# Kernel optimization log

Hardware: AMD Instinct MI355X
Metric: run time of the kernel (lower is better)

Reference implementation:

```python
import jax, jax.numpy as jnp
import numpy as np
import math

B = 128        # batch (= bipartite matching N)
L = 16         # detector layers (MAX_LAYER)
E = 768        # n_embd
D = E // 2     # RFF target_dim
H = 12         # n_head
HD = E // H    # head_size
NL = 6         # n_layer
SEQ = 12       # tokens after concats: 3+3 -> 6 -> +currentLayer -> 12
MAX_LAYER = L
LN_EPS = 1e-3  # keras LayerNormalization default


def setup_inputs() -> dict:
    key = jax.random.key(0)
    ks = jax.random.split(key, 8)
    inp = {}
    inp["X"] = jax.random.normal(ks[0], (B, L, 3), dtype=jnp.float32) * 50.0
    inp["targets"] = jax.random.normal(ks[1], (B, L, 3), dtype=jnp.float32)
    # RandomFourierFeatures params (random per-call in original; fixed here):
    # x: xmin=-160,xmax=160,n=9*1024 ; y: n=12*512 ; dE: xmin=0,xmax=230,n=2300
    specs = [(-160.0, 160.0, 9 * 1024), (-160.0, 160.0, 12 * 512), (0.0, 230.0, 2300)]
    om, ph = [], []
    for i, (xmin, xmax, n) in enumerate(specs):
        k1, k2 = jax.random.split(jax.random.fold_in(ks[2], i))
        omin = 2.0 * math.pi / (xmax - xmin)
        lo, hi = math.log(omin / n), math.log(omin)
        om.append(jnp.exp(jax.random.uniform(k1, (D,), minval=lo, maxval=hi)))
        ph.append(jax.random.uniform(k2, (D,)))  # B ~ U(0,1)*scale, scale=1
    inp["omegas"] = jnp.stack(om).astype(jnp.float32)  # (3, D)
    inp["phases"] = jnp.stack(ph).astype(jnp.float32)  # (3, D)
    # np.random.permutation per layer-step, fixed here
    inp["perms"] = jnp.stack(
        [jax.random.permutation(jax.random.fold_in(ks[3], i), B) for i in range(L - 1)]
    ).astype(jnp.int32)  # (L-1, B)
    # transformer weights (stacked over layers)
    kk = jax.random.split(ks[4], 16)
    s = 0.02
    inp["Wq"] = jax.random.normal(kk[0], (NL, E, H, HD)) * s
    inp["bq"] = jnp.zeros((NL, H, HD))
    inp["Wk"] = jax.random.normal(kk[1], (NL, E, H, HD)) * s
    inp["bk"] = jnp.zeros((NL, H, HD))
    inp["Wv"] = jax.random.normal(kk[2], (NL, E, H, HD)) * s
    inp["bv"] = jnp.zeros((NL, H, HD))
    inp["Wo"] = jax.random.normal(kk[3], (NL, H, HD, E)) * s
    inp["bo"] = jnp.zeros((NL, E))
    inp["ln1g"] = jnp.ones((NL, E)); inp["ln1b"] = jnp.zeros((NL, E))
    inp["ln2g"] = jnp.ones((NL, E)); inp["ln2b"] = jnp.zeros((NL, E))
    inp["W1"] = jax.random.normal(kk[4], (NL, E, 4 * E)) * s
    inp["b1f"] = jnp.zeros((NL, 4 * E))
    inp["W2"] = jax.random.normal(kk[5], (NL, 4 * E, E)) * s
    inp["b2f"] = jnp.zeros((NL, E))
    inp["lnfg"] = jnp.ones((E,)); inp["lnfb"] = jnp.zeros((E,))
    inp["Wout"] = jax.random.normal(kk[6], (SEQ * E, 3)) * s
    inp["bout"] = jnp.zeros((3,))
    return inp


def _ln(x, g, b):
    mu = jnp.mean(x, -1, keepdims=True)
    v = jnp.var(x, -1, keepdims=True)
    return (x - mu) * jax.lax.rsqrt(v + LN_EPS) * g + b


def _greedy_match(cost):
    """Greedy bipartite matching: sort all NxN costs ascending, assign first-come.
    Returns row_to_col_match_vec (N,) int32."""
    N = cost.shape[0]
    order = jnp.argsort(cost.reshape(-1))

    def step(carry, k):
        row, col = carry
        i = k // N
        j = k % N
        ok = (row[i] == -1) & (col[j] == -1)
        row = row.at[i].set(jnp.where(ok, j, row[i]))
        col = col.at[j].set(jnp.where(ok, i, col[j]))
        return (row, col), None

    init = (jnp.full((N,), -1, jnp.int32), jnp.full((N,), -1, jnp.int32))
    (row, _), _ = jax.lax.scan(step, init, order)
    return row


def _forward(X, targets, omegas, phases, perms, Wq, bq, Wk, bk, Wv, bv, Wo, bo,
             ln1g, ln1b, ln2g, ln2b, W1, b1f, W2, b2f, lnfg, lnfb, Wout, bout):
    # RFF: (B,L,3) -> (B,L,3,D)
    XS = jnp.cos(X[..., None] * omegas[None, None, :, :] + phases[None, None, :, :])
    losses = []
    scale = 1.0 / math.sqrt(HD)
    for lidx in range(1, L):
        xc = XS[:, -lidx]        # (B,3,D)
        xp = XS[:, -lidx - 1]    # (B,3,D)
        x = jnp.concatenate([xc, xp], axis=2)            # (B,3,E)
        y = targets[:, -lidx + 1]                        # (B,3)
        y_prev = jnp.broadcast_to(y[:, :, None], (B, 3, E))
        x = jnp.concatenate([x, y_prev], axis=1)         # (B,6,E)
        cur = jnp.full_like(x, float(MAX_LAYER - lidx))
        x = jnp.concatenate([x, cur], axis=1)            # (B,12,E)
        x = x[perms[lidx - 1]]                           # batch permutation
        for l in range(NL):
            h = _ln(x, ln1g[l], ln1b[l])
            q = jnp.einsum('bse,ehd->bshd', h, Wq[l]) + bq[l]
            k = jnp.einsum('bse,ehd->bshd', h, Wk[l]) + bk[l]
            v = jnp.einsum('bse,ehd->bshd', h, Wv[l]) + bv[l]
            att = jax.nn.softmax(jnp.einsum('bqhd,bkhd->bhqk', q, k) * scale, axis=-1)
            o = jnp.einsum('bhqk,bkhd->bqhd', att, v)
            x = x + (jnp.einsum('bqhd,hde->bqe', o, Wo[l]) + bo[l])
            h = _ln(x, ln2g[l], ln2b[l])
            x = x + (jnp.maximum(h @ W1[l] + b1f[l], 0.0) @ W2[l] + b2f[l])
        x = _ln(x, lnfg, lnfb).reshape(B, SEQ * E)
        logits = x @ Wout + bout                         # (B,3)
        tgt = targets[:, -lidx]                          # (B,3)
        cost = jnp.sqrt(jnp.sum((logits[:, None, :] - tgt[None, :, :]) ** 2, axis=-1) + 1e-12)
        m = _greedy_match(jax.lax.stop_gradient(cost))
        lm = logits[m]                                   # gather per original
        losses.append(jnp.mean((lm - tgt) ** 2))
    return jnp.mean(jnp.stack(losses))


def reference(X, targets, omegas, phases, perms, Wq, bq, Wk, bk, Wv, bv, Wo, bo,
              ln1g, ln1b, ln2g, ln2b, W1, b1f, W2, b2f, lnfg, lnfb, Wout, bout):
    return _forward(X, targets, omegas, phases, perms, Wq, bq, Wk, bk, Wv, bv, Wo, bo,
                    ln1g, ln1b, ln2g, ln2b, W1, b1f, W2, b2f, lnfg, lnfb, Wout, bout)
```

## Files before the change

kernel.cpp:

```cpp
#include <hip/hip_runtime.h>
#include <hip/hip_bf16.h>
#include <math.h>

#define B_   128
#define L_   16
#define E_   768
#define D_   384
#define H_   12
#define HD_  64
#define NL_  6
#define SEQ_ 12
#define LN_EPS 0.001f
#define WLS   7077888
#define BQS   2304

typedef __attribute__((ext_vector_type(8))) short bf16x8;
typedef __attribute__((ext_vector_type(4))) float f32x4;
typedef unsigned long long u64;

#define GLOAD_LDS16(g, l) \
    __builtin_amdgcn_global_load_lds((__attribute__((address_space(1))) const void*)(g), \
                                     (__attribute__((address_space(3))) void*)(l), 16, 0, 0)

__global__ __launch_bounds__(256) void k_x0(const float* __restrict__ X,
                                            const float* __restrict__ targets,
                                            const int* __restrict__ perms,
                                            const float* __restrict__ om,
                                            const float* __restrict__ ph,
                                            float* __restrict__ x, int cb, int ntok) {
    int i = blockIdx.x * 256 + threadIdx.x;
    if (i >= ntok*E_) return;
    int e   = i % E_;
    int tok = i / E_;
    int s   = tok % SEQ_;
    int bi  = (tok / SEQ_) % B_;
    int c   = tok / (SEQ_*B_);
    int cl  = cb + c;
    int lidx = cl + 1;
    int pb  = perms[cl*B_ + bi];
    float val;
    if (s < 3) {
        int t  = (e < D_) ? (L_ - lidx) : (L_ - lidx - 1);
        int dd = (e < D_) ? e : (e - D_);
        float xv = X[(pb*L_ + t)*3 + s];
        val = cosf(xv * om[s*D_ + dd] + ph[s*D_ + dd]);
    } else if (s < 6) {
        int t = (17 - lidx) & 15;
        val = targets[(pb*L_ + t)*3 + (s - 3)];
    } else {
        val = (float)(L_ - lidx);
    }
    x[i] = val;
}

__global__ __launch_bounds__(256) void k_ln(const float* __restrict__ x,
                                            const float* __restrict__ g,
                                            const float* __restrict__ b,
                                            __hip_bfloat16* __restrict__ h) {
    int gi = blockIdx.x * 256 + threadIdx.x;
    int tok = gi >> 6, lane = gi & 63;
    const float4* xr = (const float4*)(x + (size_t)tok * E_);
    float4 v0 = xr[lane], v1 = xr[lane + 64], v2 = xr[lane + 128];
    float s = v0.x+v0.y+v0.z+v0.w + v1.x+v1.y+v1.z+v1.w + v2.x+v2.y+v2.z+v2.w;
    #pragma unroll
    for (int o = 32; o > 0; o >>= 1) s += __shfl_xor(s, o, 64);
    float mu = s * (1.0f / E_);
    v0.x-=mu; v0.y-=mu; v0.z-=mu; v0.w-=mu;
    v1.x-=mu; v1.y-=mu; v1.z-=mu; v1.w-=mu;
    v2.x-=mu; v2.y-=mu; v2.z-=mu; v2.w-=mu;
    float q = v0.x*v0.x+v0.y*v0.y+v0.z*v0.z+v0.w*v0.w
            + v1.x*v1.x+v1.y*v1.y+v1.z*v1.z+v1.w*v1.w
            + v2.x*v2.x+v2.y*v2.y+v2.z*v2.z+v2.w*v2.w;
    #pragma unroll
    for (int o = 32; o > 0; o >>= 1) q += __shfl_xor(q, o, 64);
    float rstd = rsqrtf(q * (1.0f / E_) + LN_EPS);
    const float4* g4 = (const float4*)g;
    const float4* b4 = (const float4*)b;
    ushort4* h4 = (ushort4*)(h + (size_t)tok * E_);
    #pragma unroll
    for (int k = 0; k < 3; k++) {
        float4 v = (k == 0) ? v0 : (k == 1) ? v1 : v2;
        float4 gg = g4[lane + k*64], bb = b4[lane + k*64];
        ushort4 o;
        o.x = __bfloat16_as_ushort(__float2bfloat16(v.x * rstd * gg.x + bb.x));
        o.y = __bfloat16_as_ushort(__float2bfloat16(v.y * rstd * gg.y + bb.y));
        o.z = __bfloat16_as_ushort(__float2bfloat16(v.z * rstd * gg.z + bb.z));
        o.w = __bfloat16_as_ushort(__float2bfloat16(v.w * rstd * gg.w + bb.w));
        h4[lane + k*64] = o;
    }
}

__global__ __launch_bounds__(256) void k_cvt(const float* __restrict__ Wq,
                                             const float* __restrict__ Wk,
                                             const float* __restrict__ Wv,
                                             const float* __restrict__ Wo,
                                             const float* __restrict__ W1,
                                             const float* __restrict__ W2,
                                             const float* __restrict__ bq,
                                             const float* __restrict__ bk,
                                             const float* __restrict__ bv,
                                             __hip_bfloat16* __restrict__ wl0,
                                             float* __restrict__ bqkv0, int lbase) {
    int bid = blockIdx.x;
    int l   = lbase + bid / 6913;
    bid %= 6913;
    __hip_bfloat16* wl = wl0 + (size_t)(l - lbase) * WLS;
    float* bqkv = bqkv0 + (l - lbase) * BQS;
    int tid = threadIdx.x;
    if (bid == 6912) {
        for (int i = tid; i < 2304; i += 256) {
            float v = (i < 768) ? bq[l*768 + i] : (i < 1536) ? bk[l*768 + i - 768]
                                                             : bv[l*768 + i - 1536];
            bqkv[i] = v;
        }
        return;
    }
    const float* src; __hip_bfloat16* dst; int K, N, ti, tj;
    if (bid < 1728) {
        int part = bid / 576, idx = bid % 576;
        const float* srcs[3] = {Wq, Wk, Wv};
        src = srcs[part] + (size_t)l*768*768; dst = wl + (size_t)part*768*768;
        K = 768; N = 768; tj = idx % 24; ti = idx / 24;
    } else if (bid < 2304) {
        int idx = bid - 1728;
        src = Wo + (size_t)l*768*768; dst = wl + 1769472;
        K = 768; N = 768; tj = idx % 24; ti = idx / 24;
    } else if (bid < 4608) {
        int idx = bid - 2304;
        src = W1 + (size_t)l*768*3072; dst = wl + 2359296;
        K = 768; N = 3072; tj = idx % 96; ti = idx / 96;
    } else {
        int idx = bid - 4608;
        src = W2 + (size_t)l*3072*768; dst = wl + 4718592;
        K = 3072; N = 768; tj = idx % 24; ti = idx / 24;
    }
    __shared__ float tbuf[32][33];
    int tx = tid & 31, ty = tid >> 5;
    #pragma unroll
    for (int p = 0; p < 4; p++) {
        int k = ti*32 + ty + p*8, n = tj*32 + tx;
        tbuf[ty + p*8][tx] = src[(size_t)k*N + n];
    }
    __syncthreads();
    #pragma unroll
    for (int p = 0; p < 4; p++) {
        int n = tj*32 + ty + p*8, k = ti*32 + tx;
        dst[(size_t)n*K + k] = __float2bfloat16(tbuf[tx][ty + p*8]);
    }
}

#define MFMA_BF16(a, b, c) __builtin_amdgcn_mfma_f32_16x16x32_bf16(a, b, c, 0, 0, 0)

__global__ __launch_bounds__(512) void k_gemm256(const __hip_bfloat16* __restrict__ A,
                                                 const __hip_bfloat16* __restrict__ Bt,
                                                 const float* __restrict__ bias,
                                                 void* __restrict__ Cp,
                                                 int K, int ldb, int ldc, int flags) {
    __shared__ __align__(16) char smem[131072];
    const int tid  = threadIdx.x;
    const int lane = tid & 63;
    const int wid  = tid >> 6;
    const int wr   = wid >> 2;
    const int wc   = wid & 3;
    const int m0   = blockIdx.y * 256;
    const int n0   = blockIdx.x * 256;
    const int fr   = lane & 15, fkg = lane >> 4, sx = fr & 7;
    const int NT   = K >> 6;

    const int srow = tid >> 3;
    const int skc  = 8 * ((tid & 7) ^ (srow & 7));

    f32x4 acc[8][4] = {};

    auto stage = [&](int kt, int buf) {
        char* base = smem + buf*65536;
        const int kk = kt*64 + skc;
        GLOAD_LDS16(A  + (size_t)(m0 +       srow) * K   + kk, base +         tid*16);
        GLOAD_LDS16(A  + (size_t)(m0 +  64 + srow) * K   + kk, base +  8192 + tid*16);
        GLOAD_LDS16(A  + (size_t)(m0 + 128 + srow) * K   + kk, base + 16384 + tid*16);
        GLOAD_LDS16(A  + (size_t)(m0 + 192 + srow) * K   + kk, base + 24576 + tid*16);
        GLOAD_LDS16(Bt + (size_t)(n0 +       srow) * ldb + kk, base + 32768 + tid*16);
        GLOAD_LDS16(Bt + (size_t)(n0 +  64 + srow) * ldb + kk, base + 40960 + tid*16);
        GLOAD_LDS16(Bt + (size_t)(n0 + 128 + srow) * ldb + kk, base + 49152 + tid*16);
        GLOAD_LDS16(Bt + (size_t)(n0 + 192 + srow) * ldb + kk, base + 57344 + tid*16);
    };
    auto ldA = [&](int buf, int i, int ks) -> bf16x8 {
        int row = wr*128 + i*16 + fr;
        return *(const bf16x8*)(smem + buf*65536 + row*128 + (((ks*4 + fkg) ^ sx) << 4));
    };
    auto ldB = [&](int buf, int j, int ks) -> bf16x8 {
        int row = wc*64 + j*16 + fr;
        return *(const bf16x8*)(smem + buf*65536 + 32768 + row*128 + (((ks*4 + fkg) ^ sx) << 4));
    };

    stage(0, 0);
    __syncthreads();

    for (int kt = 0; kt < NT; ++kt) {
        const int cur = kt & 1;
        if (kt + 1 < NT) stage(kt + 1, cur ^ 1);
        bf16x8 b[4][2];
        #pragma unroll
        for (int j = 0; j < 4; j++) { b[j][0] = ldB(cur, j, 0); b[j][1] = ldB(cur, j, 1); }
        #pragma unroll
        for (int ih = 0; ih < 2; ih++) {
            bf16x8 a[4][2];
            #pragma unroll
            for (int i = 0; i < 4; i++) {
                a[i][0] = ldA(cur, ih*4 + i, 0);
                a[i][1] = ldA(cur, ih*4 + i, 1);
            }
            __builtin_amdgcn_s_setprio(1);
            #pragma unroll
            for (int i = 0; i < 4; i++)
                #pragma unroll
                for (int j = 0; j < 4; j++) {
                    acc[ih*4+i][j] = MFMA_BF16(a[i][0], b[j][0], acc[ih*4+i][j]);
                    acc[ih*4+i][j] = MFMA_BF16(a[i][1], b[j][1], acc[ih*4+i][j]);
                }
            __builtin_amdgcn_s_setprio(0);
        }
        __syncthreads();
    }

    const int colL = lane & 15, rowg = (lane >> 4) * 4;
    #pragma unroll
    for (int i = 0; i < 8; i++) {
        #pragma unroll
        for (int j = 0; j < 4; j++) {
            int col = n0 + wc*64 + j*16 + colL;
            float bv = bias ? bias[col] : 0.0f;
            #pragma unroll
            for (int r = 0; r < 4; r++) {
                int row = m0 + wr*128 + i*16 + rowg + r;
                float v = acc[i][j][r] + bv;
                if (flags & 4) v = fmaxf(v, 0.0f);
                size_t off = (size_t)row * ldc + col;
                if (flags & 1)      ((__hip_bfloat16*)Cp)[off] = __float2bfloat16(v);
                else if (flags & 2) ((float*)Cp)[off] += v;
                else                ((float*)Cp)[off] = v;
            }
        }
    }
}

__global__ __launch_bounds__(256) void k_attn(const __hip_bfloat16* __restrict__ qkv,
                                              __hip_bfloat16* __restrict__ o) {
    __shared__ float qs[SEQ_][HD_], ks[SEQ_][HD_], vs[SEQ_][HD_];
    __shared__ float att[SEQ_][SEQ_];
    int blk = blockIdx.x;
    int hh  = blk % H_;
    int cbb = blk / H_;
    int t = threadIdx.x;
    if (t < 96) {
        int s = t >> 3, c = (t & 7) * 8;
        size_t base = (size_t)(cbb*SEQ_ + s) * 2304 + hh*64 + c;
        bf16x8 q8 = *(const bf16x8*)(qkv + base);
        bf16x8 k8 = *(const bf16x8*)(qkv + base + 768);
        bf16x8 v8 = *(const bf16x8*)(qkv + base + 1536);
        #pragma unroll
        for (int j = 0; j < 8; j++) {
            qs[s][c+j] = __uint_as_float((unsigned)(unsigned short)q8[j] << 16);
            ks[s][c+j] = __uint_as_float((unsigned)(unsigned short)k8[j] << 16);
            vs[s][c+j] = __uint_as_float((unsigned)(unsigned short)v8[j] << 16);
        }
    }
    __syncthreads();
    if (t < SEQ_*SEQ_) {
        int qi = t / SEQ_, kj = t % SEQ_;
        float s = 0.f;
        #pragma unroll
        for (int d = 0; d < HD_; d++) s += qs[qi][d] * ks[kj][d];
        att[qi][kj] = s * 0.125f;
    }
    __syncthreads();
    if (t < SEQ_) {
        float mx = -1e30f;
        #pragma unroll
        for (int j = 0; j < SEQ_; j++) mx = fmaxf(mx, att[t][j]);
        float e[SEQ_]; float sum = 0.f;
        #pragma unroll
        for (int j = 0; j < SEQ_; j++) { e[j] = expf(att[t][j] - mx); sum += e[j]; }
        float inv = 1.f / sum;
        #pragma unroll
        for (int j = 0; j < SEQ_; j++) att[t][j] = e[j] * inv;
    }
    __syncthreads();
    for (int i = t; i < SEQ_*HD_; i += 256) {
        int s = i / HD_, d = i % HD_;
        float acc = 0.f;
        #pragma unroll
        for (int j = 0; j < SEQ_; j++) acc += att[s][j] * vs[j][d];
        o[(size_t)(cbb*SEQ_ + s) * 768 + hh*64 + d] = __float2bfloat16(acc);
    }
}

__global__ __launch_bounds__(256) void k_logits(const __hip_bfloat16* __restrict__ hfin,
                                                const float* __restrict__ Wout,
                                                const float* __restrict__ bout,
                                                float* __restrict__ logits, int cb) {
    __shared__ float red[3][256];
    int blk = blockIdx.x;
    int t = threadIdx.x;
    const __hip_bfloat16* row = hfin + (size_t)blk * SEQ_ * E_;
    float a0 = 0.f, a1 = 0.f, a2 = 0.f;
    for (int e = t; e < SEQ_*E_; e += 256) {
        float x = __bfloat162float(row[e]);
        a0 += x * Wout[e*3 + 0]; a1 += x * Wout[e*3 + 1]; a2 += x * Wout[e*3 + 2];
    }
    red[0][t] = a0; red[1][t] = a1; red[2][t] = a2;
    __syncthreads();
    for (int o = 128; o > 0; o >>= 1) {
        if (t < o) { red[0][t] += red[0][t+o]; red[1][t] += red[1][t+o]; red[2][t] += red[2][t+o]; }
        __syncthreads();
    }
    if (t < 3) logits[((size_t)cb*B_ + blk)*3 + t] = red[t][0] + bout[t];
}

__global__ __launch_bounds__(64) void k_match(const float* __restrict__ logits,
                                              const float* __restrict__ targets,
                                              float* __restrict__ losses) {
    __shared__ float cst[128 * 129];
    __shared__ float tg[128][3];
    __shared__ int mrow[128];
    int cl = blockIdx.x, lane = threadIdx.x;
    int lidx = cl + 1;
    for (int j = lane; j < 128; j += 64) {
        const float* tp = &targets[((size_t)j*L_ + (L_ - lidx)) * 3];
        tg[j][0] = tp[0]; tg[j][1] = tp[1]; tg[j][2] = tp[2];
    }
    __syncthreads();
    u64 kc[2];
    #pragma unroll
    for (int hh = 0; hh < 2; hh++) {
        int r = lane + hh*64;
        const float* lg = &logits[(cl*B_ + r) * 3];
        float l0 = lg[0], l1 = lg[1], l2 = lg[2];
        u64 best = ~0ull;
        for (int c = 0; c < 128; c++) {
            float d0 = l0 - tg[c][0], d1 = l1 - tg[c][1], d2 = l2 - tg[c][2];
            float cc = sqrtf(d0*d0 + d1*d1 + d2*d2 + 1e-12f);
            cst[r*129 + c] = cc;
            u64 key = ((u64)__float_as_uint(cc) << 14) | (unsigned)(r*128 + c);
            best = key < best ? key : best;
        }
        kc[hh] = best;
    }
    __syncthreads();
    u64 dead0 = 0, dead1 = 0;
    int done = 0;
    for (int trip = 0; trip < 16640 && done < 128; trip++) {
        u64 b = kc[0] < kc[1] ? kc[0] : kc[1];
        #pragma unroll
        for (int o = 32; o > 0; o >>= 1) {
            u64 x = __shfl_xor(b, o, 64);
            b = x < b ? x : b;
        }
        unsigned e  = (unsigned)b & 0x3fffu;
        unsigned wi = e >> 7, wj = e & 127;
        bool isDead = (((wj < 64) ? (dead0 >> wj) : (dead1 >> (wj - 64))) & 1ull) != 0;
        if (!isDead) {
            if ((wi & 63u) == (unsigned)lane) {
                mrow[wi] = (int)wj;
                kc[wi >> 6] = ~0ull;
            }
            if (wj < 64) dead0 |= 1ull << wj; else dead1 |= 1ull << (wj - 64);
            done++;
        } else {
            float c0 = cst[wi*129 + lane];
            float c1 = cst[wi*129 + lane + 64];
            bool d0b = ((dead0 >> lane) & 1ull) != 0;
            bool d1b = ((dead1 >> lane) & 1ull) != 0;
            u64 k0 = d0b ? ~0ull : (((u64)__float_as_uint(c0) << 14) | (unsigned)(wi*128 + lane));
            u64 k1 = d1b ? ~0ull : (((u64)__float_as_uint(c1) << 14) | (unsigned)(wi*128 + lane + 64));
            u64 nb = k0 < k1 ? k0 : k1;
            #pragma unroll
            for (int o = 32; o > 0; o >>= 1) {
                u64 x = __shfl_xor(nb, o, 64);
                nb = x < nb ? x : nb;
            }
            if ((wi & 63u) == (unsigned)lane) kc[wi >> 6] = nb;
        }
    }
    __syncthreads();
    float a = 0.f;
    #pragma unroll
    for (int hh = 0; hh < 2; hh++) {
        int r = lane + hh*64;
        const float* lg = &logits[(cl*B_ + mrow[r]) * 3];
        float d0 = lg[0]-tg[r][0], d1 = lg[1]-tg[r][1], d2 = lg[2]-tg[r][2];
        a += d0*d0 + d1*d1 + d2*d2;
    }
    #pragma unroll
    for (int o = 32; o > 0; o >>= 1) a += __shfl_xor(a, o, 64);
    if (lane == 0) losses[cl] = a * (1.0f / (B_*3));
}

__global__ void k_final(const float* __restrict__ losses, float* __restrict__ out) {
    float s = 0.f;
    for (int i = 0; i < 15; i++) s += losses[i];
    out[0] = s * (1.0f / 15.0f);
}

extern "C" void kernel_launch(void* const* d_in, const int* in_sizes, int n_in,
                              void* d_out, int out_size, void* d_ws, size_t ws_size,
                              hipStream_t stream) {
    (void)in_sizes; (void)n_in; (void)out_size;
    const float* X       = (const float*)d_in[0];
    const float* targets = (const float*)d_in[1];
    const float* omegas  = (const float*)d_in[2];
    const float* phases  = (const float*)d_in[3];
    const int*   perms   = (const int*)d_in[4];
    const float* Wq  = (const float*)d_in[5];
    const float* bq  = (const float*)d_in[6];
    const float* Wk  = (const float*)d_in[7];
    const float* bk  = (const float*)d_in[8];
    const float* Wv  = (const float*)d_in[9];
    const float* bv  = (const float*)d_in[10];
    const float* Wo  = (const float*)d_in[11];
    const float* bo  = (const float*)d_in[12];
    const float* ln1g = (const float*)d_in[13];
    const float* ln1b = (const float*)d_in[14];
    const float* ln2g = (const float*)d_in[15];
    const float* ln2b = (const float*)d_in[16];
    const float* W1  = (const float*)d_in[17];
    const float* b1f = (const float*)d_in[18];
    const float* W2  = (const float*)d_in[19];
    const float* b2f = (const float*)d_in[20];
    const float* lnfg = (const float*)d_in[21];
    const float* lnfb = (const float*)d_in[22];
    const float* Wout = (const float*)d_in[23];
    const float* bout = (const float*)d_in[24];

    int CL; bool hoist;
    if (ws_size >= 263000000ull)      { CL = 15; hoist = false; }
    else if (ws_size >= 169000000ull) { CL = 5;  hoist = true;  }
    else                              { CL = 5;  hoist = false; }
    int M = CL * B_ * SEQ_;
    bool perLayerCvt = (CL == 15) || !hoist;

    char* wsb = (char*)d_ws;
    size_t off = 0;
    auto alloc = [&](size_t bytes) {
        char* p = wsb + off;
        off += (bytes + 255) & ~(size_t)255;
        return p;
    };
    float*          x      = (float*)alloc((size_t)M*E_*4);
    __hip_bfloat16* h      = (__hip_bfloat16*)alloc((size_t)M*E_*2);
    __hip_bfloat16* qkvh   = (__hip_bfloat16*)alloc((size_t)M*3072*2);
    __hip_bfloat16* wl     = (__hip_bfloat16*)alloc((hoist ? 6 : 1) * (size_t)WLS*2);
    float*          bqkv   = (float*)alloc((hoist ? 6 : 1) * (size_t)BQS*4);
    float*          logits = (float*)alloc(23040);
    float*          losses = (float*)alloc(64);

    if (hoist)
        k_cvt<<<6*6913, 256, 0, stream>>>(Wq, Wk, Wv, Wo, W1, W2, bq, bk, bv, wl, bqkv, 0);

    dim3 gQKV(2304/256, M/256);
    dim3 gF1 (3072/256, M/256);
    dim3 gN  (768/256,  M/256);
    dim3 gLN (M/4);

    for (int cb = 0; cb < 15; cb += CL) {
        k_x0<<<(M*E_)/256, 256, 0, stream>>>(X, targets, perms, omegas, phases, x, cb, M);
        for (int l = 0; l < NL_; l++) {
            __hip_bfloat16* wlp = hoist ? wl + (size_t)l*WLS : wl;
            float*          bqp = hoist ? bqkv + l*BQS : bqkv;
            if (perLayerCvt)
                k_cvt<<<6913, 256, 0, stream>>>(Wq, Wk, Wv, Wo, W1, W2, bq, bk, bv, wlp, bqp, l);
            k_ln<<<gLN, 256, 0, stream>>>(x, ln1g + l*E_, ln1b + l*E_, h);
            k_gemm256<<<gQKV, 512, 0, stream>>>(h, wlp, bqp, qkvh, 768, 768, 2304, 1);
            k_attn<<<CL*B_*H_, 256, 0, stream>>>(qkvh, h);
            k_gemm256<<<gN, 512, 0, stream>>>(h, wlp + 1769472, bo + l*E_, x,
                                              768, 768, 768, 2);
            k_ln<<<gLN, 256, 0, stream>>>(x, ln2g + l*E_, ln2b + l*E_, h);
            k_gemm256<<<gF1, 512, 0, stream>>>(h, wlp + 2359296, b1f + l*3072, qkvh,
                                               768, 768, 3072, 1|4);
            k_gemm256<<<gN, 512, 0, stream>>>(qkvh, wlp + 4718592, b2f + l*E_, x,
                                              3072, 3072, 768, 2);
        }
        k_ln<<<gLN, 256, 0, stream>>>(x, lnfg, lnfb, h);
        k_logits<<<CL*B_, 256, 0, stream>>>(h, Wout, bout, logits, cb);
    }
    k_match<<<15, 64, 0, stream>>>(logits, targets, losses);
    k_final<<<1, 1, 0, stream>>>(losses, (float*)d_out);
}
```

Baseline: 5.097 ms.

## Add 128x128 GEMM for narrow N=768 projections and XCD-aware block swizzle

Adds a 128x128-tile GEMM kernel with 256 threads and uses it for the attention output projection and the second FFN projection, where N=768 left the 256-tile grid with too few workgroups. It also remaps the flat block index so that consecutive tiles land on the same XCD, improving L2 reuse in both GEMM kernels. The smaller tiles lower per-block arithmetic intensity and add more global traffic in exchange for better CU occupancy.

```diff
diff --git a/kernel.cpp b/kernel.cpp
--- a/kernel.cpp
+++ b/kernel.cpp
@@ -162,8 +162,16 @@
     const int wid  = tid >> 6;
     const int wr   = wid >> 2;
     const int wc   = wid & 3;
-    const int m0   = blockIdx.y * 256;
-    const int n0   = blockIdx.x * 256;
+
+    const int gx   = gridDim.x;
+    const int nwg  = gx * gridDim.y;
+    const int flat = blockIdx.y * gx + blockIdx.x;
+    const int q8   = nwg >> 3, r8 = nwg & 7;
+    const int xcd  = flat & 7, off8 = flat >> 3;
+    const int swz  = (xcd < r8 ? xcd*(q8+1) : r8*(q8+1) + (xcd-r8)*q8) + off8;
+    const int m0   = (swz / gx) * 256;
+    const int n0   = (swz % gx) * 256;
+
     const int fr   = lane & 15, fkg = lane >> 4, sx = fr & 7;
     const int NT   = K >> 6;
 
@@ -233,6 +241,100 @@
             #pragma unroll
             for (int r = 0; r < 4; r++) {
                 int row = m0 + wr*128 + i*16 + rowg + r;
+                float v = acc[i][j][r] + bv;
+                if (flags & 4) v = fmaxf(v, 0.0f);
+                size_t off = (size_t)row * ldc + col;
+                if (flags & 1)      ((__hip_bfloat16*)Cp)[off] = __float2bfloat16(v);
+                else if (flags & 2) ((float*)Cp)[off] += v;
+                else                ((float*)Cp)[off] = v;
+            }
+        }
+    }
+}
+
+__global__ __launch_bounds__(256) void k_gemm128(const __hip_bfloat16* __restrict__ A,
+                                                 const __hip_bfloat16* __restrict__ Bt,
+                                                 const float* __restrict__ bias,
+                                                 void* __restrict__ Cp,
+                                                 int K, int ldb, int ldc, int flags) {
+    __shared__ __align__(16) char smem[65536];
+    const int tid  = threadIdx.x;
+    const int lane = tid & 63;
+    const int wid  = tid >> 6;
+    const int wr   = wid >> 1;
+    const int wc   = wid & 1;
+
+    const int gx   = gridDim.x;
+    const int nwg  = gx * gridDim.y;
+    const int flat = blockIdx.y * gx + blockIdx.x;
+    const int q8   = nwg >> 3, r8 = nwg & 7;
+    const int xcd  = flat & 7, off8 = flat >> 3;
+    const int swz  = (xcd < r8 ? xcd*(q8+1) : r8*(q8+1) + (xcd-r8)*q8) + off8;
+    const int m0   = (swz / gx) * 128;
+    const int n0   = (swz % gx) * 128;
+
+    const int fr   = lane & 15, fkg = lane >> 4, sx = fr & 7;
+    const int NT   = K >> 6;
+
+    const int srow = tid >> 3;
+    const int skc  = 8 * ((tid & 7) ^ (srow & 7));
+
+    f32x4 acc[4][4] = {};
+
+    auto stage = [&](int kt, int buf) {
+        char* base = smem + buf*32768;
+        const int kk = kt*64 + skc;
+        GLOAD_LDS16(A  + (size_t)(m0 +      srow) * K   + kk, base +         tid*16);
+        GLOAD_LDS16(A  + (size_t)(m0 + 32 + srow) * K   + kk, base +  4096 + tid*16);
+        GLOAD_LDS16(A  + (size_t)(m0 + 64 + srow) * K   + kk, base +  8192 + tid*16);
+        GLOAD_LDS16(A  + (size_t)(m0 + 96 + srow) * K   + kk, base + 12288 + tid*16);
+        GLOAD_LDS16(Bt + (size_t)(n0 +      srow) * ldb + kk, base + 16384 + tid*16);
+        GLOAD_LDS16(Bt + (size_t)(n0 + 32 + srow) * ldb + kk, base + 20480 + tid*16);
+        GLOAD_LDS16(Bt + (size_t)(n0 + 64 + srow) * ldb + kk, base + 24576 + tid*16);
+        GLOAD_LDS16(Bt + (size_t)(n0 + 96 + srow) * ldb + kk, base + 28672 + tid*16);
+    };
+    auto ldA = [&](int buf, int i, int ks) -> bf16x8 {
+        int row = wr*64 + i*16 + fr;
+        return *(const bf16x8*)(smem + buf*32768 + row*128 + (((ks*4 + fkg) ^ sx) << 4));
+    };
+    auto ldB = [&](int buf, int j, int ks) -> bf16x8 {
+        int row = wc*64 + j*16 + fr;
+        return *(const bf16x8*)(smem + buf*32768 + 16384 + row*128 + (((ks*4 + fkg) ^ sx) << 4));
+    };
+
+    stage(0, 0);
+    __syncthreads();
+
+    for (int kt = 0; kt < NT; ++kt) {
+        const int cur = kt & 1;
+        if (kt + 1 < NT) stage(kt + 1, cur ^ 1);
+        bf16x8 b[4][2], a[4][2];
+        #pragma unroll
+        for (int j = 0; j < 4; j++) { b[j][0] = ldB(cur, j, 0); b[j][1] = ldB(cur, j, 1); }
+        #pragma unroll
+        for (int i = 0; i < 4; i++) { a[i][0] = ldA(cur, i, 0); a[i][1] = ldA(cur, i, 1); }
+        __builtin_amdgcn_s_setprio(1);
+        #pragma unroll
+        for (int i = 0; i < 4; i++)
+            #pragma unroll
+            for (int j = 0; j < 4; j++) {
+                acc[i][j] = MFMA_BF16(a[i][0], b[j][0], acc[i][j]);
+                acc[i][j] = MFMA_BF16(a[i][1], b[j][1], acc[i][j]);
+            }
+        __builtin_amdgcn_s_setprio(0);
+        __syncthreads();
+    }
+
+    const int colL = lane & 15, rowg = (lane >> 4) * 4;
+    #pragma unroll
+    for (int i = 0; i < 4; i++) {
+        #pragma unroll
+        for (int j = 0; j < 4; j++) {
+            int col = n0 + wc*64 + j*16 + colL;
+            float bv = bias ? bias[col] : 0.0f;
+            #pragma unroll
+            for (int r = 0; r < 4; r++) {
+                int row = m0 + wr*64 + i*16 + rowg + r;
                 float v = acc[i][j][r] + bv;
                 if (flags & 4) v = fmaxf(v, 0.0f);
                 size_t off = (size_t)row * ldc + col;
@@ -459,7 +561,7 @@
 
     dim3 gQKV(2304/256, M/256);
     dim3 gF1 (3072/256, M/256);
-    dim3 gN  (768/256,  M/256);
+    dim3 gN  (768/128,  M/128);
     dim3 gLN (M/4);
 
     for (int cb = 0; cb < 15; cb += CL) {
@@ -472,12 +574,12 @@
             k_ln<<<gLN, 256, 0, stream>>>(x, ln1g + l*E_, ln1b + l*E_, h);
             k_gemm256<<<gQKV, 512, 0, stream>>>(h, wlp, bqp, qkvh, 768, 768, 2304, 1);
             k_attn<<<CL*B_*H_, 256, 0, stream>>>(qkvh, h);
-            k_gemm256<<<gN, 512, 0, stream>>>(h, wlp + 1769472, bo + l*E_, x,
+            k_gemm128<<<gN, 256, 0, stream>>>(h, wlp + 1769472, bo + l*E_, x,
                                               768, 768, 768, 2);
             k_ln<<<gLN, 256, 0, stream>>>(x, ln2g + l*E_, ln2b + l*E_, h);
             k_gemm256<<<gF1, 512, 0, stream>>>(h, wlp + 2359296, b1f + l*3072, qkvh,
                                                768, 768, 3072, 1|4);
-            k_gemm256<<<gN, 512, 0, stream>>>(qkvh, wlp + 4718592, b2f + l*E_, x,
+            k_gemm128<<<gN, 256, 0, stream>>>(qkvh, wlp + 4718592, b2f + l*E_, x,
                                               3072, 3072, 768, 2);
         }
         k_ln<<<gLN, 256, 0, stream>>>(x, lnfg, lnfb, h);
```

After: 4.555 ms. 1.12x faster.

## Shrink GEMM tiles to 128x128 with XCD-aware block swizzle

Applied to the files above, without the earlier changes.

Replaces the 256x256 GEMM tile (512 threads, 128KB LDS) with a 128x128 tile using 256 threads and 64KB LDS, and quadruples the grid. It adds a block-index remap so consecutive tiles land on the same XCD, aiming for better L2 sharing. The smaller tile raises workgroup count and occupancy for the modest M, especially the N=768 GEMMs, but lowers per-block data reuse and arithmetic intensity.

```diff
diff --git a/kernel.cpp b/kernel.cpp
--- a/kernel.cpp
+++ b/kernel.cpp
@@ -151,46 +151,54 @@
 
 #define MFMA_BF16(a, b, c) __builtin_amdgcn_mfma_f32_16x16x32_bf16(a, b, c, 0, 0, 0)
 
-__global__ __launch_bounds__(512) void k_gemm256(const __hip_bfloat16* __restrict__ A,
+__global__ __launch_bounds__(256) void k_gemm128(const __hip_bfloat16* __restrict__ A,
                                                  const __hip_bfloat16* __restrict__ Bt,
                                                  const float* __restrict__ bias,
                                                  void* __restrict__ Cp,
                                                  int K, int ldb, int ldc, int flags) {
-    __shared__ __align__(16) char smem[131072];
+    __shared__ __align__(16) char smem[65536];
     const int tid  = threadIdx.x;
     const int lane = tid & 63;
     const int wid  = tid >> 6;
-    const int wr   = wid >> 2;
-    const int wc   = wid & 3;
-    const int m0   = blockIdx.y * 256;
-    const int n0   = blockIdx.x * 256;
+    const int wr   = wid >> 1;
+    const int wc   = wid & 1;
+
+    const int gx   = gridDim.x;
+    const int nwg  = gx * gridDim.y;
+    const int flat = blockIdx.y * gx + blockIdx.x;
+    const int q8   = nwg >> 3, r8 = nwg & 7;
+    const int xcd  = flat & 7, off8 = flat >> 3;
+    const int swz  = (xcd < r8 ? xcd*(q8+1) : r8*(q8+1) + (xcd-r8)*q8) + off8;
+    const int m0   = (swz / gx) * 128;
+    const int n0   = (swz % gx) * 128;
+
     const int fr   = lane & 15, fkg = lane >> 4, sx = fr & 7;
     const int NT   = K >> 6;
 
     const int srow = tid >> 3;
     const int skc  = 8 * ((tid & 7) ^ (srow & 7));
 
-    f32x4 acc[8][4] = {};
+    f32x4 acc[4][4] = {};
 
     auto stage = [&](int kt, int buf) {
-        char* base = smem + buf*65536;
+        char* base = smem + buf*32768;
         const int kk = kt*64 + skc;
-        GLOAD_LDS16(A  + (size_t)(m0 +       srow) * K   + kk, base +         tid*16);
-        GLOAD_LDS16(A  + (size_t)(m0 +  64 + srow) * K   + kk, base +  8192 + tid*16);
-        GLOAD_LDS16(A  + (size_t)(m0 + 128 + srow) * K   + kk, base + 16384 + tid*16);
-        GLOAD_LDS16(A  + (size_t)(m0 + 192 + srow) * K   + kk, base + 24576 + tid*16);
-        GLOAD_LDS16(Bt + (size_t)(n0 +       srow) * ldb + kk, base + 32768 + tid*16);
-        GLOAD_LDS16(Bt + (size_t)(n0 +  64 + srow) * ldb + kk, base + 40960 + tid*16);
-        GLOAD_LDS16(Bt + (size_t)(n0 + 128 + srow) * ldb + kk, base + 49152 + tid*16);
-        GLOAD_LDS16(Bt + (size_t)(n0 + 192 + srow) * ldb + kk, base + 57344 + tid*16);
+        GLOAD_LDS16(A  + (size_t)(m0 +      srow) * K   + kk, base +         tid*16);
+        GLOAD_LDS16(A  + (size_t)(m0 + 32 + srow) * K   + kk, base +  4096 + tid*16);
+        GLOAD_LDS16(A  + (size_t)(m0 + 64 + srow) * K   + kk, base +  8192 + tid*16);
+        GLOAD_LDS16(A  + (size_t)(m0 + 96 + srow) * K   + kk, base + 12288 + tid*16);
+        GLOAD_LDS16(Bt + (size_t)(n0 +      srow) * ldb + kk, base + 16384 + tid*16);
+        GLOAD_LDS16(Bt + (size_t)(n0 + 32 + srow) * ldb + kk, base + 20480 + tid*16);
+        GLOAD_LDS16(Bt + (size_t)(n0 + 64 + srow) * ldb + kk, base + 24576 + tid*16);
+        GLOAD_LDS16(Bt + (size_t)(n0 + 96 + srow) * ldb + kk, base + 28672 + tid*16);
     };
     auto ldA = [&](int buf, int i, int ks) -> bf16x8 {
-        int row = wr*128 + i*16 + fr;
-        return *(const bf16x8*)(smem + buf*65536 + row*128 + (((ks*4 + fkg) ^ sx) << 4));
+        int row = wr*64 + i*16 + fr;
+        return *(const bf16x8*)(smem + buf*32768 + row*128 + (((ks*4 + fkg) ^ sx) << 4));
     };
     auto ldB = [&](int buf, int j, int ks) -> bf16x8 {
         int row = wc*64 + j*16 + fr;
-        return *(const bf16x8*)(smem + buf*65536 + 32768 + row*128 + (((ks*4 + fkg) ^ sx) << 4));
+        return *(const bf16x8*)(smem + buf*32768 + 16384 + row*128 + (((ks*4 + fkg) ^ sx) << 4));
     };
 
     stage(0, 0);
@@ -199,40 +207,33 @@
     for (int kt = 0; kt < NT; ++kt) {
         const int cur = kt & 1;
         if (kt + 1 < NT) stage(kt + 1, cur ^ 1);
-        bf16x8 b[4][2];
+        bf16x8 b[4][2], a[4][2];
         #pragma unroll
         for (int j = 0; j < 4; j++) { b[j][0] = ldB(cur, j, 0); b[j][1] = ldB(cur, j, 1); }
         #pragma unroll
-        for (int ih = 0; ih < 2; ih++) {
-            bf16x8 a[4][2];
+        for (int i = 0; i < 4; i++) { a[i][0] = ldA(cur, i, 0); a[i][1] = ldA(cur, i, 1); }
+        __builtin_amdgcn_s_setprio(1);
+        #pragma unroll
+        for (int i = 0; i < 4; i++)
             #pragma unroll
-            for (int i = 0; i < 4; i++) {
-                a[i][0] = ldA(cur, ih*4 + i, 0);
-                a[i][1] = ldA(cur, ih*4 + i, 1);
+            for (int j = 0; j < 4; j++) {
+                acc[i][j] = MFMA_BF16(a[i][0], b[j][0], acc[i][j]);
+                acc[i][j] = MFMA_BF16(a[i][1], b[j][1], acc[i][j]);
             }
-            __builtin_amdgcn_s_setprio(1);
-            #pragma unroll
-            for (int i = 0; i < 4; i++)
-                #pragma unroll
-                for (int j = 0; j < 4; j++) {
-                    acc[ih*4+i][j] = MFMA_BF16(a[i][0], b[j][0], acc[ih*4+i][j]);
-                    acc[ih*4+i][j] = MFMA_BF16(a[i][1], b[j][1], acc[ih*4+i][j]);
-                }
-            __builtin_amdgcn_s_setprio(0);
-        }
+        __builtin_amdgcn_s_setprio(0);
         __syncthreads();
     }
 
     const int colL = lane & 15, rowg = (lane >> 4) * 4;
     #pragma unroll
-    for (int i = 0; i < 8; i++) {
+    for (int i = 0; i < 4; i++) {
         #pragma unroll
         for (int j = 0; j < 4; j++) {
             int col = n0 + wc*64 + j*16 + colL;
             float bv = bias ? bias[col] : 0.0f;
             #pragma unroll
             for (int r = 0; r < 4; r++) {
-                int row = m0 + wr*128 + i*16 + rowg + r;
+                int row = m0 + wr*64 + i*16 + rowg + r;
                 float v = acc[i][j][r] + bv;
                 if (flags & 4) v = fmaxf(v, 0.0f);
                 size_t off = (size_t)row * ldc + col;
@@ -457,9 +458,9 @@
     if (hoist)
         k_cvt<<<6*6913, 256, 0, stream>>>(Wq, Wk, Wv, Wo, W1, W2, bq, bk, bv, wl, bqkv, 0);
 
-    dim3 gQKV(2304/256, M/256);
-    dim3 gF1 (3072/256, M/256);
-    dim3 gN  (768/256,  M/256);
+    dim3 gQKV(2304/128, M/128);
+    dim3 gF1 (3072/128, M/128);
+    dim3 gN  (768/128,  M/128);
     dim3 gLN (M/4);
 
     for (int cb = 0; cb < 15; cb += CL) {
@@ -470,14 +471,14 @@
             if (perLayerCvt)
                 k_cvt<<<6913, 256, 0, stream>>>(Wq, Wk, Wv, Wo, W1, W2, bq, bk, bv, wlp, bqp, l);
             k_ln<<<gLN, 256, 0, stream>>>(x, ln1g + l*E_, ln1b + l*E_, h);
-            k_gemm256<<<gQKV, 512, 0, stream>>>(h, wlp, bqp, qkvh, 768, 768, 2304, 1);
+            k_gemm128<<<gQKV, 256, 0, stream>>>(h, wlp, bqp, qkvh, 768, 768, 2304, 1);
             k_attn<<<CL*B_*H_, 256, 0, stream>>>(qkvh, h);
-            k_gemm256<<<gN, 512, 0, stream>>>(h, wlp + 1769472, bo + l*E_, x,
+            k_gemm128<<<gN, 256, 0, stream>>>(h, wlp + 1769472, bo + l*E_, x,
                                               768, 768, 768, 2);
             k_ln<<<gLN, 256, 0, stream>>>(x, ln2g + l*E_, ln2b + l*E_, h);
-            k_gemm256<<<gF1, 512, 0, stream>>>(h, wlp + 2359296, b1f + l*3072, qkvh,
+            k_gemm128<<<gF1, 256, 0, stream>>>(h, wlp + 2359296, b1f + l*3072, qkvh,
                                                768, 768, 3072, 1|4);
-            k_gemm256<<<gN, 512, 0, stream>>>(qkvh, wlp + 4718592, b2f + l*E_, x,
+            k_gemm128<<<gN, 256, 0, stream>>>(qkvh, wlp + 4718592, b2f + l*E_, x,
                                               3072, 3072, 768, 2);
         }
         k_ln<<<gLN, 256, 0, stream>>>(x, lnfg, lnfb, h);
```

New measurement: 4.515 ms. 1.13x faster.
